# Optimization experiments

Measured on AMD Instinct MI355X. Metric: run time of the kernel, lower is better.

Reference implementation:

```python
import jax, jax.numpy as jnp
import numpy as np

B, H, G, EPG = 32768, 4096, 16, 16
E = G * EPG  # 256 total experts
STD = 0.02


def setup_inputs() -> dict:
    key = jax.random.key(0)
    k1, k2, k3 = jax.random.split(key, 3)
    hidden_states = jax.random.normal(k1, (B, H), dtype=jnp.float32)
    group_w = STD * jax.random.normal(k2, (G, H), dtype=jnp.float32)   # group_router.weight
    expert_w = STD * jax.random.normal(k3, (G, EPG, H), dtype=jnp.float32)  # stacked expert_routers[g].weight
    return {"hidden_states": hidden_states, "group_w": group_w, "expert_w": expert_w}


def reference(hidden_states, group_w, expert_w):
    b, h = hidden_states.shape
    g, epg, _ = expert_w.shape
    e = g * epg

    # Level 1: group routing (argmax of softmax == argmax of logits)
    group_logits = hidden_states @ group_w.T                      # [B, G]
    selected_groups = jnp.argmax(group_logits, axis=-1)           # [B]

    # Level 2: expert logits for every group, then gather the selected group's block.
    # (Math identical to per-token loop computing only the selected group's router.)
    logits_all = jnp.einsum('bh,geh->bge', hidden_states, expert_w)  # [B, G, EPG]
    sel_logits = jnp.take_along_axis(
        logits_all, selected_groups[:, None, None], axis=1)[:, 0, :]  # [B, EPG]

    expert_probs = jax.nn.softmax(sel_logits, axis=-1)            # [B, EPG]
    local_idx = jnp.argmax(expert_probs, axis=-1)                 # [B]
    selected_experts = selected_groups * epg + local_idx          # [B]
    expert_weights = jnp.take_along_axis(expert_probs, local_idx[:, None], axis=1)[:, 0]  # [B]

    # Scatter the selected group's logits into the global [B, E] tensor (rest zero).
    rows = jnp.arange(b)[:, None]                                 # [B, 1]
    cols = selected_groups[:, None] * epg + jnp.arange(epg)[None, :]  # [B, EPG]
    all_expert_logits = jnp.zeros((b, e), dtype=hidden_states.dtype).at[rows, cols].set(sel_logits)

    return all_expert_logits, selected_experts[:, None], expert_weights[:, None]
```

## Files before the change

kernel.cpp:

```cpp
#include <hip/hip_runtime.h>


constexpr int Btok = 32768;
constexpr int Hdim = 4096;
constexpr int Gn   = 16;
constexpr int EPGn = 16;
constexpr int En   = 256;
constexpr int WV   = 16;
constexpr int Hs   = Hdim / WV;
constexpr int TILE = 1024;

__global__ __launch_bounds__(1024, 8) void k_group(
    const float* __restrict__ hidden, const float* __restrict__ gw,
    unsigned char* __restrict__ gsel)
{
  const int lane = threadIdx.x & 63;
  const int wq = __builtin_amdgcn_readfirstlane((int)(threadIdx.x >> 6));
  const int token = blockIdx.x * 64 + lane;
  const float* hrow  = hidden + (size_t)token * Hdim + wq * Hs;
  const float* wbase = gw + wq * Hs;

  float acc[Gn];
#pragma unroll
  for (int g = 0; g < Gn; ++g) acc[g] = 0.f;

#pragma unroll 2
  for (int j = 0; j < Hs; j += 4) {
    const float4 h4 = *reinterpret_cast<const float4*>(hrow + j);
#pragma unroll
    for (int g = 0; g < Gn; ++g) {
      const float* wg = wbase + g * Hdim + j;
      acc[g] += h4.x * wg[0] + h4.y * wg[1] + h4.z * wg[2] + h4.w * wg[3];
    }
  }

  __shared__ float part[8][64][Gn + 1];
  if (wq >= 8) {
#pragma unroll
    for (int g = 0; g < Gn; ++g) part[wq - 8][lane][g] = acc[g];
  }
  __syncthreads();
  if (wq < 8) {
#pragma unroll
    for (int g = 0; g < Gn; ++g) part[wq][lane][g] += acc[g];
  }
  __syncthreads();

  const int tok = threadIdx.x >> 4;
  const int g   = threadIdx.x & 15;
  float v = 0.f;
#pragma unroll
  for (int s = 0; s < 8; ++s) v += part[s][tok][g];

  int bi = g;
#pragma unroll
  for (int off = 8; off; off >>= 1) {
    float v2 = __shfl_xor(v, off);
    int   i2 = __shfl_xor(bi, off);
    if (v2 > v || (v2 == v && i2 < bi)) { v = v2; bi = i2; }
  }
  if (g == 0) gsel[blockIdx.x * 64 + tok] = (unsigned char)bi;
}

__global__ __launch_bounds__(1024, 8) void k_expert(
    const float* __restrict__ hidden, const float* __restrict__ ew,
    const unsigned char* __restrict__ gsel,
    float* __restrict__ out0,
    float* __restrict__ out1,
    float* __restrict__ out2)
{
  const int g = blockIdx.x;
  const int tbase = blockIdx.y * TILE;

  __shared__ int   list[TILE];
  __shared__ int   cnt;
  __shared__ float part[8][64][EPGn + 1];
  __shared__ float lrow[64][EPGn + 1];

  if (threadIdx.x == 0) cnt = 0;
  __syncthreads();
  for (int i = threadIdx.x; i < TILE; i += 1024) {
    if ((int)gsel[tbase + i] == g) {
      int p = atomicAdd(&cnt, 1);
      list[p] = tbase + i;
    }
  }
  __syncthreads();
  const int n = cnt;

  const int lane = threadIdx.x & 63;
  const int wq = __builtin_amdgcn_readfirstlane((int)(threadIdx.x >> 6));
  const float* wbase = ew + ((size_t)g * EPGn) * Hdim + wq * Hs;

  for (int s0 = 0; s0 < n; s0 += 64) {
    const int ns = min(64, n - s0);
    const int token = list[s0 + ((lane < ns) ? lane : 0)];
    const float* hrow = hidden + (size_t)token * Hdim + wq * Hs;

    float acc[EPGn];
#pragma unroll
    for (int e = 0; e < EPGn; ++e) acc[e] = 0.f;

#pragma unroll 2
    for (int j = 0; j < Hs; j += 4) {
      const float4 h4 = *reinterpret_cast<const float4*>(hrow + j);
#pragma unroll
      for (int e = 0; e < EPGn; ++e) {
        const float* we = wbase + e * Hdim + j;
        acc[e] += h4.x * we[0] + h4.y * we[1] + h4.z * we[2] + h4.w * we[3];
      }
    }

    if (wq >= 8) {
#pragma unroll
      for (int e = 0; e < EPGn; ++e) part[wq - 8][lane][e] = acc[e];
    }
    __syncthreads();
    if (wq < 8) {
#pragma unroll
      for (int e = 0; e < EPGn; ++e) part[wq][lane][e] += acc[e];
    }
    __syncthreads();

    const int tk = threadIdx.x >> 4;
    const int e  = threadIdx.x & 15;
    float l = 0.f;
#pragma unroll
    for (int s = 0; s < 8; ++s) l += part[s][tk][e];
    lrow[tk][e] = l;

    float m = l;
#pragma unroll
    for (int off = 8; off; off >>= 1) m = fmaxf(m, __shfl_xor(m, off));
    float sum = __expf(l - m);
#pragma unroll
    for (int off = 8; off; off >>= 1) sum += __shfl_xor(sum, off);

    float v = l; int bi = e;
#pragma unroll
    for (int off = 8; off; off >>= 1) {
      float v2 = __shfl_xor(v, off);
      int   i2 = __shfl_xor(bi, off);
      if (v2 > v || (v2 == v && i2 < bi)) { v = v2; bi = i2; }
    }
    if (e == 0 && tk < ns) {
      const int tok = list[s0 + tk];
      out1[tok] = (float)(g * EPGn + bi);
      out2[tok] = 1.f / sum;
    }

    const int r = tk;
    const int p = e;
    if (r < ns) {
      const int tok = list[s0 + r];
      float* row = out0 + (size_t)tok * En + p * 16;
      if (p == g) {
#pragma unroll
        for (int q = 0; q < 4; ++q) {
          float4 v4;
          v4.x = lrow[r][q * 4 + 0];
          v4.y = lrow[r][q * 4 + 1];
          v4.z = lrow[r][q * 4 + 2];
          v4.w = lrow[r][q * 4 + 3];
          *reinterpret_cast<float4*>(row + q * 4) = v4;
        }
      } else {
        const float4 z = {0.f, 0.f, 0.f, 0.f};
#pragma unroll
        for (int q = 0; q < 4; ++q)
          *reinterpret_cast<float4*>(row + q * 4) = z;
      }
    }
    __syncthreads();
  }
}

extern "C" void kernel_launch(void* const* d_in, const int* in_sizes, int n_in,
                              void* d_out, int out_size, void* d_ws, size_t ws_size,
                              hipStream_t stream) {
  const float* hidden = (const float*)d_in[0];
  const float* gw     = (const float*)d_in[1];
  const float* ew     = (const float*)d_in[2];
  float* out0 = (float*)d_out;
  unsigned char* gsel = (unsigned char*)d_ws;

  k_group<<<Btok / 64, 1024, 0, stream>>>(hidden, gw, gsel);

  float* out1 = out0 + (size_t)Btok * En;
  float* out2 = out1 + Btok;
  k_expert<<<dim3(Gn, Btok / TILE), 1024, 0, stream>>>(
      hidden, ew, gsel, out0, out1, out2);
}
```

Measured before the change: 1.187 ms.

## Stage hidden rows through double-buffered LDS tiles with coalesced loads

Both kernels now load 64 tokens by 64 columns of hidden states per step using coalesced float4 loads. The tile is stored transposed in a double-buffered shared-memory buffer, so each wave reads its four columns across all 64 tokens. Before, each lane streamed its own row with strided per-lane loads. The next chunk is prefetched into registers while the current one is computed. The cost is a block-wide barrier per 64-column chunk (64 per pass) plus extra LDS traffic, and the larger LDS footprint may limit occupancy.

```diff
diff --git a/kernel.cpp b/kernel.cpp
--- a/kernel.cpp
+++ b/kernel.cpp
@@ -6,35 +6,64 @@
 constexpr int Gn   = 16;
 constexpr int EPGn = 16;
 constexpr int En   = 256;
-constexpr int WV   = 16;
-constexpr int Hs   = Hdim / WV;
+constexpr int BK   = 64;
+constexpr int NCH  = Hdim / BK;
 constexpr int TILE = 1024;
+
+#define AT(b,c,r) smem[(b)*(BK*65) + (c)*65 + (r)]
 
 __global__ __launch_bounds__(1024, 8) void k_group(
     const float* __restrict__ hidden, const float* __restrict__ gw,
     unsigned char* __restrict__ gsel)
 {
+  __shared__ float smem[8704];
+  float (*part)[64][Gn + 1] = reinterpret_cast<float (*)[64][Gn + 1]>(smem);
+
   const int lane = threadIdx.x & 63;
   const int wq = __builtin_amdgcn_readfirstlane((int)(threadIdx.x >> 6));
-  const int token = blockIdx.x * 64 + lane;
-  const float* hrow  = hidden + (size_t)token * Hdim + wq * Hs;
-  const float* wbase = gw + wq * Hs;
+  const int cw = wq * 4;
+  const int r  = threadIdx.x >> 4;
+  const int c0 = (threadIdx.x & 15) << 2;
+  const int tbase = blockIdx.x * 64;
+
+  const float* gptr = hidden + (size_t)(tbase + r) * Hdim + c0;
+
+  {
+    const float4 v = *reinterpret_cast<const float4*>(gptr);
+    AT(0, c0 + 0, r) = v.x; AT(0, c0 + 1, r) = v.y;
+    AT(0, c0 + 2, r) = v.z; AT(0, c0 + 3, r) = v.w;
+  }
+  __syncthreads();
 
   float acc[Gn];
 #pragma unroll
   for (int g = 0; g < Gn; ++g) acc[g] = 0.f;
 
 #pragma unroll 2
-  for (int j = 0; j < Hs; j += 4) {
-    const float4 h4 = *reinterpret_cast<const float4*>(hrow + j);
+  for (int k = 0; k < NCH; ++k) {
+    const int buf = k & 1;
+    const bool more = (k + 1 < NCH);
+    float4 p;
+    if (more) p = *reinterpret_cast<const float4*>(gptr + (k + 1) * BK);
+
+    const float a0 = AT(buf, cw + 0, lane);
+    const float a1 = AT(buf, cw + 1, lane);
+    const float a2 = AT(buf, cw + 2, lane);
+    const float a3 = AT(buf, cw + 3, lane);
+    const float* wk = gw + k * BK + cw;
 #pragma unroll
     for (int g = 0; g < Gn; ++g) {
-      const float* wg = wbase + g * Hdim + j;
-      acc[g] += h4.x * wg[0] + h4.y * wg[1] + h4.z * wg[2] + h4.w * wg[3];
-    }
-  }
-
-  __shared__ float part[8][64][Gn + 1];
+      const float* wg = wk + (size_t)g * Hdim;
+      acc[g] += a0 * wg[0] + a1 * wg[1] + a2 * wg[2] + a3 * wg[3];
+    }
+
+    if (more) {
+      AT(buf ^ 1, c0 + 0, r) = p.x; AT(buf ^ 1, c0 + 1, r) = p.y;
+      AT(buf ^ 1, c0 + 2, r) = p.z; AT(buf ^ 1, c0 + 3, r) = p.w;
+    }
+    __syncthreads();
+  }
+
   if (wq >= 8) {
 #pragma unroll
     for (int g = 0; g < Gn; ++g) part[wq - 8][lane][g] = acc[g];
@@ -59,7 +88,7 @@
     int   i2 = __shfl_xor(bi, off);
     if (v2 > v || (v2 == v && i2 < bi)) { v = v2; bi = i2; }
   }
-  if (g == 0) gsel[blockIdx.x * 64 + tok] = (unsigned char)bi;
+  if (g == 0) gsel[tbase + tok] = (unsigned char)bi;
 }
 
 __global__ __launch_bounds__(1024, 8) void k_expert(
@@ -72,10 +101,11 @@
   const int g = blockIdx.x;
   const int tbase = blockIdx.y * TILE;
 
+  __shared__ float smem[8704];
   __shared__ int   list[TILE];
   __shared__ int   cnt;
-  __shared__ float part[8][64][EPGn + 1];
   __shared__ float lrow[64][EPGn + 1];
+  float (*part)[64][EPGn + 1] = reinterpret_cast<float (*)[64][EPGn + 1]>(smem);
 
   if (threadIdx.x == 0) cnt = 0;
   __syncthreads();
@@ -90,25 +120,50 @@
 
   const int lane = threadIdx.x & 63;
   const int wq = __builtin_amdgcn_readfirstlane((int)(threadIdx.x >> 6));
-  const float* wbase = ew + ((size_t)g * EPGn) * Hdim + wq * Hs;
+  const int cw = wq * 4;
+  const int r  = threadIdx.x >> 4;
+  const int c0 = (threadIdx.x & 15) << 2;
+  const float* wbase = ew + ((size_t)g * EPGn) * Hdim;
 
   for (int s0 = 0; s0 < n; s0 += 64) {
     const int ns = min(64, n - s0);
-    const int token = list[s0 + ((lane < ns) ? lane : 0)];
-    const float* hrow = hidden + (size_t)token * Hdim + wq * Hs;
+    const int rr = (r < ns) ? r : (ns - 1);
+    const float* gptr = hidden + (size_t)list[s0 + rr] * Hdim + c0;
+
+    {
+      const float4 v = *reinterpret_cast<const float4*>(gptr);
+      AT(0, c0 + 0, r) = v.x; AT(0, c0 + 1, r) = v.y;
+      AT(0, c0 + 2, r) = v.z; AT(0, c0 + 3, r) = v.w;
+    }
+    __syncthreads();
 
     float acc[EPGn];
 #pragma unroll
     for (int e = 0; e < EPGn; ++e) acc[e] = 0.f;
 
 #pragma unroll 2
-    for (int j = 0; j < Hs; j += 4) {
-      const float4 h4 = *reinterpret_cast<const float4*>(hrow + j);
+    for (int k = 0; k < NCH; ++k) {
+      const int buf = k & 1;
+      const bool more = (k + 1 < NCH);
+      float4 p;
+      if (more) p = *reinterpret_cast<const float4*>(gptr + (k + 1) * BK);
+
+      const float a0 = AT(buf, cw + 0, lane);
+      const float a1 = AT(buf, cw + 1, lane);
+      const float a2 = AT(buf, cw + 2, lane);
+      const float a3 = AT(buf, cw + 3, lane);
+      const float* wk = wbase + k * BK + cw;
 #pragma unroll
       for (int e = 0; e < EPGn; ++e) {
-        const float* we = wbase + e * Hdim + j;
-        acc[e] += h4.x * we[0] + h4.y * we[1] + h4.z * we[2] + h4.w * we[3];
+        const float* we = wk + (size_t)e * Hdim;
+        acc[e] += a0 * we[0] + a1 * we[1] + a2 * we[2] + a3 * we[3];
       }
+
+      if (more) {
+        AT(buf ^ 1, c0 + 0, r) = p.x; AT(buf ^ 1, c0 + 1, r) = p.y;
+        AT(buf ^ 1, c0 + 2, r) = p.z; AT(buf ^ 1, c0 + 3, r) = p.w;
+      }
+      __syncthreads();
     }
 
     if (wq >= 8) {
@@ -149,19 +204,17 @@
       out2[tok] = 1.f / sum;
     }
 
-    const int r = tk;
-    const int p = e;
-    if (r < ns) {
-      const int tok = list[s0 + r];
-      float* row = out0 + (size_t)tok * En + p * 16;
-      if (p == g) {
+    if (tk < ns) {
+      const int tok = list[s0 + tk];
+      float* row = out0 + (size_t)tok * En + e * 16;
+      if (e == g) {
 #pragma unroll
         for (int q = 0; q < 4; ++q) {
           float4 v4;
-          v4.x = lrow[r][q * 4 + 0];
-          v4.y = lrow[r][q * 4 + 1];
-          v4.z = lrow[r][q * 4 + 2];
-          v4.w = lrow[r][q * 4 + 3];
+          v4.x = lrow[tk][q * 4 + 0];
+          v4.y = lrow[tk][q * 4 + 1];
+          v4.z = lrow[tk][q * 4 + 2];
+          v4.w = lrow[tk][q * 4 + 3];
           *reinterpret_cast<float4*>(row + q * 4) = v4;
         }
       } else {
```

Result: slower. 1.406 ms (+18.4%).
